# Kernel tuning notes

Measured on AMD Instinct MI355X. Metric: run time of the kernel, lower is better.

## Reference

```python
import jax, jax.numpy as jnp
import numpy as np

NUM_HEADS = 12


def setup_inputs() -> dict:
    key = jax.random.key(0)
    ks = jax.random.split(key, 4)
    N, L, C = 32, 577, 768  # L = 24*24 patches + 1 cls token
    x = jax.random.normal(ks[0], (N, L, C), dtype=jnp.float32)
    w_qkv = jax.random.normal(ks[1], (3 * C, C), dtype=jnp.float32) * 0.02
    w_proj = jax.random.normal(ks[2], (C, C), dtype=jnp.float32) * 0.02
    b_proj = jnp.zeros((C,), dtype=jnp.float32)
    w_dwc = jax.random.normal(ks[3], (C, 1, 3, 3), dtype=jnp.float32) * 0.02
    b_dwc = jnp.zeros((C,), dtype=jnp.float32)
    return {"x": x, "w_qkv": w_qkv, "w_proj": w_proj, "b_proj": b_proj,
            "w_dwc": w_dwc, "b_dwc": b_dwc}


def reference(x, w_qkv, w_proj, b_proj, w_dwc, b_dwc):
    N, L, C = x.shape
    H = NUM_HEADS
    hd = C // H
    h = w = int(L ** 0.5)  # 24; h*w == L-1 (cls token excluded)

    # qkv transform: (N, L, 3C) -> (3, N, H, L, hd)
    qkv = (x @ w_qkv.T).reshape(N, L, 3, H, hd).transpose(2, 0, 3, 1, 4)
    q, k, v = qkv[0], qkv[1], qkv[2]

    # graph-candidate attention (default: scaled dot-product softmax)
    scale = hd ** -0.5
    scores = jnp.einsum('bhqd,bhkd->bhqk', q, k) * scale
    attn = jax.nn.softmax(scores, axis=-1)
    out = jnp.einsum('bhqk,bhkd->bhqd', attn, v)  # (N, H, L, hd)
    out = out.transpose(0, 2, 1, 3).reshape(N, L, C)

    # depthwise conv on v (patch tokens only), NCHW layout
    v_ = v[:, :, 1:, :].transpose(0, 2, 1, 3).reshape(N, h, w, C).transpose(0, 3, 1, 2)
    dwc = jax.lax.conv_general_dilated(
        v_, w_dwc, window_strides=(1, 1), padding=((1, 1), (1, 1)),
        dimension_numbers=('NCHW', 'OIHW', 'NCHW'), feature_group_count=C)
    dwc = dwc + b_dwc[None, :, None, None]
    dwc = dwc.transpose(0, 2, 3, 1).reshape(N, L - 1, C)

    out = out.at[:, 1:, :].add(dwc)
    out = out @ w_proj.T + b_proj
    return out
```

## Files before the change

kernel.cpp:

```cpp
#include <hip/hip_runtime.h>

typedef short bf16x8 __attribute__((ext_vector_type(8)));
typedef float f32x4 __attribute__((ext_vector_type(4)));
typedef unsigned short u16;

#define NB 32
#define LSEQ 577
#define CD 768
#define NH 12
#define HD 64
#define MROWS (NB * LSEQ)
#define LPAD 584

#define GLD16(g, l)                                                    \
  __builtin_amdgcn_global_load_lds(                                    \
      (const __attribute__((address_space(1))) void*)(g),              \
      (__attribute__((address_space(3))) void*)(l), 16, 0, 0)

__device__ __forceinline__ u16 f2bf(float f) {
  union { float f; unsigned u; } v; v.f = f;
  unsigned u = v.u + 0x7fffu + ((v.u >> 16) & 1u);
  return (u16)(u >> 16);
}
__device__ __forceinline__ float bf2f(u16 s) {
  union { unsigned u; float f; } v; v.u = ((unsigned)s) << 16;
  return v.f;
}

__global__ __launch_bounds__(256) void cvt_bf16(
    const float* __restrict__ src, u16* __restrict__ dst, int n4) {
  int i = blockIdx.x * 256 + threadIdx.x;
  if (i < n4) {
    float4 v = reinterpret_cast<const float4*>(src)[i];
    ushort4 o;
    o.x = f2bf(v.x); o.y = f2bf(v.y); o.z = f2bf(v.z); o.w = f2bf(v.w);
    reinterpret_cast<ushort4*>(dst)[i] = o;
  }
}

__global__ __launch_bounds__(256) void qkv_gemm(
    const u16* __restrict__ xb, const u16* __restrict__ wqb,
    u16* __restrict__ qb, u16* __restrict__ kb, u16* __restrict__ vtb) {
  __shared__ __align__(16) u16 As[128 * 32];
  __shared__ __align__(16) u16 Bs[128 * 32];
  const int m0 = blockIdx.x * 128;
  const int n0 = blockIdx.y * 128;
  const int t = threadIdx.x;
  const int lane = t & 63, wid = t >> 6;
  const int wm = wid >> 1, wn = wid & 1;
  const int g = lane >> 4, cl = lane & 15;

  const int srow = wid * 32 + (lane >> 2);
  const int scol = (lane & 3) * 8;
  int ga0 = m0 + srow;      ga0 = ga0 < MROWS ? ga0 : MROWS - 1;
  int ga1 = m0 + srow + 16; ga1 = ga1 < MROWS ? ga1 : MROWS - 1;
  const u16* asrc0 = xb + (size_t)ga0 * CD + scol;
  const u16* asrc1 = xb + (size_t)ga1 * CD + scol;
  const u16* bsrc0 = wqb + (size_t)(n0 + srow) * CD + scol;
  const u16* bsrc1 = wqb + (size_t)(n0 + srow + 16) * CD + scol;
  u16* adst0 = &As[wid * 1024];
  u16* adst1 = &As[wid * 1024 + 512];
  u16* bdst0 = &Bs[wid * 1024];
  u16* bdst1 = &Bs[wid * 1024 + 512];

  const f32x4 fz = {0.f, 0.f, 0.f, 0.f};
  f32x4 acc[4][4];
#pragma unroll
  for (int i = 0; i < 4; ++i)
#pragma unroll
    for (int j = 0; j < 4; ++j) acc[i][j] = fz;

  for (int k0 = 0; k0 < CD; k0 += 32) {
    GLD16(asrc0 + k0, adst0);
    GLD16(asrc1 + k0, adst1);
    GLD16(bsrc0 + k0, bdst0);
    GLD16(bsrc1 + k0, bdst1);
    __syncthreads();
    bf16x8 af[4], bfv[4];
#pragma unroll
    for (int mt = 0; mt < 4; ++mt)
      af[mt] = *reinterpret_cast<const bf16x8*>(&As[(wm * 64 + mt * 16 + cl) * 32 + g * 8]);
#pragma unroll
    for (int nt = 0; nt < 4; ++nt)
      bfv[nt] = *reinterpret_cast<const bf16x8*>(&Bs[(wn * 64 + nt * 16 + cl) * 32 + g * 8]);
#pragma unroll
    for (int mt = 0; mt < 4; ++mt)
#pragma unroll
      for (int nt = 0; nt < 4; ++nt)
        acc[mt][nt] = __builtin_amdgcn_mfma_f32_16x16x32_bf16(af[mt], bfv[nt], acc[mt][nt], 0, 0, 0);
    __syncthreads();
  }

  const int which = n0 / CD;
  const int rem0 = n0 % CD;
#pragma unroll
  for (int mt = 0; mt < 4; ++mt) {
#pragma unroll
    for (int nt = 0; nt < 4; ++nt) {
      int n = rem0 + wn * 64 + nt * 16 + cl;
      int hh = n >> 6, d = n & 63;
#pragma unroll
      for (int r = 0; r < 4; ++r) {
        int m = m0 + wm * 64 + mt * 16 + g * 4 + r;
        if (m < MROWS) {
          int nb = m / LSEQ, l = m % LSEQ;
          if (which == 0)
            qb[(((size_t)nb * NH + hh) * LSEQ + l) * HD + d] = f2bf(acc[mt][nt][r] * 0.125f);
          else if (which == 1)
            kb[(((size_t)nb * NH + hh) * LSEQ + l) * HD + d] = f2bf(acc[mt][nt][r]);
          else
            vtb[(((size_t)nb * NH + hh) * HD + d) * LPAD + l] = f2bf(acc[mt][nt][r]);
        }
      }
    }
  }
}

__global__ __launch_bounds__(256) void attn_fwd(
    const u16* __restrict__ q, const u16* __restrict__ k,
    const u16* __restrict__ vt, u16* __restrict__ y) {
  __shared__ __align__(16) u16 Ks[64 * 72];
  __shared__ __align__(16) u16 Vts[64 * 72];
  __shared__ __align__(16) u16 Ps[4][16 * 72];

  const int qtile = blockIdx.x;
  const int h = blockIdx.y;
  const int nb = blockIdx.z;
  const int t = threadIdx.x;
  const int lane = t & 63, wid = t >> 6;
  const int g = lane >> 4, cl = lane & 15;

  const size_t hoff = ((size_t)nb * NH + h) * LSEQ * HD;
  const u16* qh = q + hoff;
  const u16* kh = k + hoff;
  const u16* vth = vt + ((size_t)nb * NH + h) * HD * LPAD;

  const int qbase = qtile * 64;
  const int qrow = qbase + wid * 16 + cl;
  const int qrc = qrow < LSEQ ? qrow : LSEQ - 1;
  bf16x8 qf0 = *reinterpret_cast<const bf16x8*>(qh + (size_t)qrc * HD + g * 8);
  bf16x8 qf1 = *reinterpret_cast<const bf16x8*>(qh + (size_t)qrc * HD + 32 + g * 8);

  const f32x4 fz = {0.f, 0.f, 0.f, 0.f};
  float mrow = -3.0e38f, lrow = 0.f;
  f32x4 oaccT[4];
#pragma unroll
  for (int dt = 0; dt < 4; ++dt) oaccT[dt] = fz;

  for (int kv = 0; kv < LSEQ; kv += 64) {
#pragma unroll
    for (int i = 0; i < 2; ++i) {
      int cidx = t + 256 * i;
      int row = cidx >> 3, c8 = (cidx & 7) << 3;
      int grow = kv + row;
      uint4 kd = {0, 0, 0, 0};
      if (grow < LSEQ) kd = *reinterpret_cast<const uint4*>(kh + (size_t)grow * HD + c8);
      *reinterpret_cast<uint4*>(&Ks[row * 72 + c8]) = kd;
      uint4 vd = *reinterpret_cast<const uint4*>(vth + (size_t)row * LPAD + kv + c8);
      *reinterpret_cast<uint4*>(&Vts[row * 72 + c8]) = vd;
    }
    __syncthreads();

    f32x4 sT[4];
#pragma unroll
    for (int nt = 0; nt < 4; ++nt) {
      bf16x8 a0 = *reinterpret_cast<const bf16x8*>(&Ks[(nt * 16 + cl) * 72 + g * 8]);
      bf16x8 a1 = *reinterpret_cast<const bf16x8*>(&Ks[(nt * 16 + cl) * 72 + 32 + g * 8]);
      f32x4 s = fz;
      s = __builtin_amdgcn_mfma_f32_16x16x32_bf16(a0, qf0, s, 0, 0, 0);
      s = __builtin_amdgcn_mfma_f32_16x16x32_bf16(a1, qf1, s, 0, 0, 0);
      sT[nt] = s;
    }

#pragma unroll
    for (int nt = 0; nt < 4; ++nt)
#pragma unroll
      for (int r = 0; r < 4; ++r)
        if (kv + nt * 16 + g * 4 + r >= LSEQ) sT[nt][r] = -3.0e38f;

    float pm = -3.0e38f;
#pragma unroll
    for (int nt = 0; nt < 4; ++nt)
#pragma unroll
      for (int r = 0; r < 4; ++r) pm = fmaxf(pm, sT[nt][r]);
    pm = fmaxf(pm, __shfl_xor(pm, 16));
    pm = fmaxf(pm, __shfl_xor(pm, 32));

    float nm = fmaxf(mrow, pm);
    float alpha = __expf(mrow - nm);
    mrow = nm;
    float ps = 0.f;
#pragma unroll
    for (int nt = 0; nt < 4; ++nt)
#pragma unroll
      for (int r = 0; r < 4; ++r) {
        float p = __expf(sT[nt][r] - nm);
        sT[nt][r] = p;
        ps += p;
      }
    ps += __shfl_xor(ps, 16);
    ps += __shfl_xor(ps, 32);
    lrow = lrow * alpha + ps;
#pragma unroll
    for (int dt = 0; dt < 4; ++dt) oaccT[dt] *= alpha;

#pragma unroll
    for (int nt = 0; nt < 4; ++nt) {
      ushort4 p4;
      p4.x = f2bf(sT[nt][0]); p4.y = f2bf(sT[nt][1]);
      p4.z = f2bf(sT[nt][2]); p4.w = f2bf(sT[nt][3]);
      *reinterpret_cast<ushort4*>(&Ps[wid][cl * 72 + nt * 16 + g * 4]) = p4;
    }
    __syncthreads();

#pragma unroll
    for (int kc = 0; kc < 2; ++kc) {
      bf16x8 pa = *reinterpret_cast<const bf16x8*>(&Ps[wid][cl * 72 + kc * 32 + g * 8]);
#pragma unroll
      for (int dt = 0; dt < 4; ++dt) {
        bf16x8 va = *reinterpret_cast<const bf16x8*>(&Vts[(dt * 16 + cl) * 72 + kc * 32 + g * 8]);
        oaccT[dt] = __builtin_amdgcn_mfma_f32_16x16x32_bf16(va, pa, oaccT[dt], 0, 0, 0);
      }
    }
    __syncthreads();
  }

  if (qrow < LSEQ) {
    float inv = 1.f / lrow;
#pragma unroll
    for (int dt = 0; dt < 4; ++dt) {
      ushort4 o4;
      o4.x = f2bf(oaccT[dt][0] * inv); o4.y = f2bf(oaccT[dt][1] * inv);
      o4.z = f2bf(oaccT[dt][2] * inv); o4.w = f2bf(oaccT[dt][3] * inv);
      *reinterpret_cast<ushort4*>(
          &y[((size_t)nb * LSEQ + qrow) * CD + h * HD + dt * 16 + g * 4]) = o4;
    }
  }
}

__global__ __launch_bounds__(256) void dwc_add(
    const u16* __restrict__ vt, const float* __restrict__ wd,
    const float* __restrict__ bd, u16* __restrict__ y) {
  __shared__ u16 V[32 * 588];
  const int d0 = blockIdx.x * 32;
  const int h = blockIdx.y;
  const int nb = blockIdx.z;
  const int t = threadIdx.x;
  const u16* vrow = vt + (((size_t)nb * NH + h) * HD + d0) * LPAD;

  for (int c = t; c < 32 * 73; c += 256) {
    int row = c / 73;
    int k0 = (c - row * 73) * 8;
    uint4 vv = *reinterpret_cast<const uint4*>(vrow + (size_t)row * LPAD + k0);
    const u16* vp = (const u16*)&vv;
    *reinterpret_cast<ushort4*>(&V[row * 588 + k0]) = *(const ushort4*)vp;
    *reinterpret_cast<ushort4*>(&V[row * 588 + k0 + 4]) = *(const ushort4*)(vp + 4);
  }
  __syncthreads();

  const int d = t & 31;
  const int c = h * HD + d0 + d;
  float w9[9];
#pragma unroll
  for (int j = 0; j < 9; ++j) w9[j] = wd[c * 9 + j];
  const float bias = bd[c];
  const u16* Vd = &V[d * 588];

  for (int it = 0; it < 72; ++it) {
    int li = (t >> 5) + it * 8;
    int py = li / 24, px = li - py * 24;
    float acc = bias;
#pragma unroll
    for (int ky = 0; ky < 3; ++ky) {
      int yy = py + ky - 1;
      if (yy < 0 || yy >= 24) continue;
      int base = 1 + yy * 24;
#pragma unroll
      for (int kx = 0; kx < 3; ++kx) {
        int xx = px + kx - 1;
        if (xx < 0 || xx >= 24) continue;
        acc += w9[ky * 3 + kx] * bf2f(Vd[base + xx]);
      }
    }
    size_t yi = ((size_t)nb * LSEQ + 1 + li) * CD + c;
    y[yi] = f2bf(bf2f(y[yi]) + acc);
  }
}

__global__ __launch_bounds__(256) void proj_gemm(
    const u16* __restrict__ yb, const u16* __restrict__ wpb,
    const float* __restrict__ bias, float* __restrict__ out) {
  __shared__ __align__(16) u16 As[128 * 32];
  __shared__ __align__(16) u16 Bs[128 * 32];
  const int m0 = blockIdx.x * 128;
  const int n0 = blockIdx.y * 128;
  const int t = threadIdx.x;
  const int lane = t & 63, wid = t >> 6;
  const int wm = wid >> 1, wn = wid & 1;
  const int g = lane >> 4, cl = lane & 15;

  const int srow = wid * 32 + (lane >> 2);
  const int scol = (lane & 3) * 8;
  int ga0 = m0 + srow;      ga0 = ga0 < MROWS ? ga0 : MROWS - 1;
  int ga1 = m0 + srow + 16; ga1 = ga1 < MROWS ? ga1 : MROWS - 1;
  const u16* asrc0 = yb + (size_t)ga0 * CD + scol;
  const u16* asrc1 = yb + (size_t)ga1 * CD + scol;
  const u16* bsrc0 = wpb + (size_t)(n0 + srow) * CD + scol;
  const u16* bsrc1 = wpb + (size_t)(n0 + srow + 16) * CD + scol;
  u16* adst0 = &As[wid * 1024];
  u16* adst1 = &As[wid * 1024 + 512];
  u16* bdst0 = &Bs[wid * 1024];
  u16* bdst1 = &Bs[wid * 1024 + 512];

  const f32x4 fz = {0.f, 0.f, 0.f, 0.f};
  f32x4 acc[4][4];
#pragma unroll
  for (int i = 0; i < 4; ++i)
#pragma unroll
    for (int j = 0; j < 4; ++j) acc[i][j] = fz;

  for (int k0 = 0; k0 < CD; k0 += 32) {
    GLD16(asrc0 + k0, adst0);
    GLD16(asrc1 + k0, adst1);
    GLD16(bsrc0 + k0, bdst0);
    GLD16(bsrc1 + k0, bdst1);
    __syncthreads();
    bf16x8 af[4], bfv[4];
#pragma unroll
    for (int mt = 0; mt < 4; ++mt)
      af[mt] = *reinterpret_cast<const bf16x8*>(&As[(wm * 64 + mt * 16 + cl) * 32 + g * 8]);
#pragma unroll
    for (int nt = 0; nt < 4; ++nt)
      bfv[nt] = *reinterpret_cast<const bf16x8*>(&Bs[(wn * 64 + nt * 16 + cl) * 32 + g * 8]);
#pragma unroll
    for (int mt = 0; mt < 4; ++mt)
#pragma unroll
      for (int nt = 0; nt < 4; ++nt)
        acc[mt][nt] = __builtin_amdgcn_mfma_f32_16x16x32_bf16(af[mt], bfv[nt], acc[mt][nt], 0, 0, 0);
    __syncthreads();
  }

#pragma unroll
  for (int nt = 0; nt < 4; ++nt) {
    int n = n0 + wn * 64 + nt * 16 + cl;
    float bn = bias[n];
#pragma unroll
    for (int mt = 0; mt < 4; ++mt)
#pragma unroll
      for (int r = 0; r < 4; ++r) {
        int m = m0 + wm * 64 + mt * 16 + g * 4 + r;
        if (m < MROWS) out[(size_t)m * CD + n] = acc[mt][nt][r] + bn;
      }
  }
}

extern "C" void kernel_launch(void* const* d_in, const int* in_sizes, int n_in,
                              void* d_out, int out_size, void* d_ws, size_t ws_size,
                              hipStream_t stream) {
  const float* x = (const float*)d_in[0];
  const float* w_qkv = (const float*)d_in[1];
  const float* w_proj = (const float*)d_in[2];
  const float* b_proj = (const float*)d_in[3];
  const float* w_dwc = (const float*)d_in[4];
  const float* b_dwc = (const float*)d_in[5];
  float* out = (float*)d_out;

  const size_t SEG = (size_t)NB * NH * LSEQ * HD;
  const size_t SEGT = (size_t)NB * NH * HD * LPAD;
  const size_t YN = (size_t)MROWS * CD;
  u16* yb = (u16*)d_ws;
  u16* xb = yb;
  u16* qb = yb + YN;
  u16* kb = qb + SEG;
  u16* vtb = kb + SEG;
  u16* wqb = vtb + SEGT;
  u16* wpb = wqb + (size_t)3 * CD * CD;

  cvt_bf16<<<dim3((int)(YN / 4 / 256)), 256, 0, stream>>>(x, xb, (int)(YN / 4));
  cvt_bf16<<<dim3(3 * CD * CD / 4 / 256), 256, 0, stream>>>(w_qkv, wqb, 3 * CD * CD / 4);
  cvt_bf16<<<dim3(CD * CD / 4 / 256), 256, 0, stream>>>(w_proj, wpb, CD * CD / 4);
  qkv_gemm<<<dim3(145, 18), 256, 0, stream>>>(xb, wqb, qb, kb, vtb);
  attn_fwd<<<dim3(10, 12, 32), 256, 0, stream>>>(qb, kb, vtb, yb);
  dwc_add<<<dim3(2, 12, 32), 256, 0, stream>>>(vtb, w_dwc, b_dwc, yb);
  proj_gemm<<<dim3(145, 6), 256, 0, stream>>>(yb, wpb, b_proj, out);
}
```

Before: 404.0 us.

## Double-buffer LDS in both GEMMs and enlarge QKV tile to 256x256

Both GEMM kernels now keep two LDS buffers and issue the async global-to-LDS loads for the next K slice before running the MFMAs on the current one, with s_setprio raised around the MFMA block. This leaves one barrier per iteration and lets load latency overlap with math. The QKV GEMM also moves to 256x256 tiles with 512 threads (8 waves, 128x64 per wave), which raises operand reuse per LDS load and cuts the grid to 73x9 blocks. In exchange it uses more registers and LDS per block and leaves fewer blocks, so tail effects on the 18464-row M dimension may matter.

Result: no change. 397.3 us (-1.6%).

```diff
diff --git a/kernel.cpp b/kernel.cpp
--- a/kernel.cpp
+++ b/kernel.cpp
@@ -38,72 +38,82 @@
   }
 }
 
-__global__ __launch_bounds__(256) void qkv_gemm(
+__global__ __launch_bounds__(512, 2) void qkv_gemm(
     const u16* __restrict__ xb, const u16* __restrict__ wqb,
     u16* __restrict__ qb, u16* __restrict__ kb, u16* __restrict__ vtb) {
-  __shared__ __align__(16) u16 As[128 * 32];
-  __shared__ __align__(16) u16 Bs[128 * 32];
-  const int m0 = blockIdx.x * 128;
-  const int n0 = blockIdx.y * 128;
+  __shared__ __align__(16) u16 As[2][256 * 32];
+  __shared__ __align__(16) u16 Bs[2][256 * 32];
+  const int m0 = blockIdx.x * 256;
+  const int n0 = blockIdx.y * 256;
   const int t = threadIdx.x;
   const int lane = t & 63, wid = t >> 6;
-  const int wm = wid >> 1, wn = wid & 1;
+  const int wm = wid >> 2, wn = wid & 3;
   const int g = lane >> 4, cl = lane & 15;
 
-  const int srow = wid * 32 + (lane >> 2);
+  const int r16 = lane >> 2;
   const int scol = (lane & 3) * 8;
-  int ga0 = m0 + srow;      ga0 = ga0 < MROWS ? ga0 : MROWS - 1;
-  int ga1 = m0 + srow + 16; ga1 = ga1 < MROWS ? ga1 : MROWS - 1;
-  const u16* asrc0 = xb + (size_t)ga0 * CD + scol;
-  const u16* asrc1 = xb + (size_t)ga1 * CD + scol;
-  const u16* bsrc0 = wqb + (size_t)(n0 + srow) * CD + scol;
-  const u16* bsrc1 = wqb + (size_t)(n0 + srow + 16) * CD + scol;
-  u16* adst0 = &As[wid * 1024];
-  u16* adst1 = &As[wid * 1024 + 512];
-  u16* bdst0 = &Bs[wid * 1024];
-  u16* bdst1 = &Bs[wid * 1024 + 512];
+  const int ra0 = wid * 16 + r16;
+  const int ra1 = 128 + wid * 16 + r16;
+  int gm0 = m0 + ra0; gm0 = gm0 < MROWS ? gm0 : MROWS - 1;
+  int gm1 = m0 + ra1; gm1 = gm1 < MROWS ? gm1 : MROWS - 1;
+  const u16* ax0 = xb + (size_t)gm0 * CD + scol;
+  const u16* ax1 = xb + (size_t)gm1 * CD + scol;
+  const u16* bx0 = wqb + (size_t)(n0 + ra0) * CD + scol;
+  const u16* bx1 = wqb + (size_t)(n0 + ra1) * CD + scol;
 
   const f32x4 fz = {0.f, 0.f, 0.f, 0.f};
-  f32x4 acc[4][4];
-#pragma unroll
-  for (int i = 0; i < 4; ++i)
+  f32x4 acc[8][4];
+#pragma unroll
+  for (int i = 0; i < 8; ++i)
 #pragma unroll
     for (int j = 0; j < 4; ++j) acc[i][j] = fz;
 
-  for (int k0 = 0; k0 < CD; k0 += 32) {
-    GLD16(asrc0 + k0, adst0);
-    GLD16(asrc1 + k0, adst1);
-    GLD16(bsrc0 + k0, bdst0);
-    GLD16(bsrc1 + k0, bdst1);
-    __syncthreads();
-    bf16x8 af[4], bfv[4];
-#pragma unroll
-    for (int mt = 0; mt < 4; ++mt)
-      af[mt] = *reinterpret_cast<const bf16x8*>(&As[(wm * 64 + mt * 16 + cl) * 32 + g * 8]);
+#define QSTAGE(b, kt)                                  \
+  do {                                                 \
+    int kc = (kt) * 32;                                \
+    GLD16(ax0 + kc, &As[b][wid * 512]);                \
+    GLD16(ax1 + kc, &As[b][(wid + 8) * 512]);          \
+    GLD16(bx0 + kc, &Bs[b][wid * 512]);                \
+    GLD16(bx1 + kc, &Bs[b][(wid + 8) * 512]);          \
+  } while (0)
+
+  QSTAGE(0, 0);
+  __syncthreads();
+  int cur = 0;
+  for (int kt = 0; kt < 24; ++kt) {
+    if (kt < 23) QSTAGE(cur ^ 1, kt + 1);
+    bf16x8 af[8], bfv[4];
+#pragma unroll
+    for (int mt = 0; mt < 8; ++mt)
+      af[mt] = *reinterpret_cast<const bf16x8*>(&As[cur][(wm * 128 + mt * 16 + cl) * 32 + g * 8]);
 #pragma unroll
     for (int nt = 0; nt < 4; ++nt)
-      bfv[nt] = *reinterpret_cast<const bf16x8*>(&Bs[(wn * 64 + nt * 16 + cl) * 32 + g * 8]);
-#pragma unroll
-    for (int mt = 0; mt < 4; ++mt)
+      bfv[nt] = *reinterpret_cast<const bf16x8*>(&Bs[cur][(wn * 64 + nt * 16 + cl) * 32 + g * 8]);
+    __builtin_amdgcn_s_setprio(1);
+#pragma unroll
+    for (int mt = 0; mt < 8; ++mt)
 #pragma unroll
       for (int nt = 0; nt < 4; ++nt)
         acc[mt][nt] = __builtin_amdgcn_mfma_f32_16x16x32_bf16(af[mt], bfv[nt], acc[mt][nt], 0, 0, 0);
+    __builtin_amdgcn_s_setprio(0);
     __syncthreads();
-  }
+    cur ^= 1;
+  }
+#undef QSTAGE
 
   const int which = n0 / CD;
   const int rem0 = n0 % CD;
 #pragma unroll
-  for (int mt = 0; mt < 4; ++mt) {
+  for (int mt = 0; mt < 8; ++mt) {
 #pragma unroll
     for (int nt = 0; nt < 4; ++nt) {
-      int n = rem0 + wn * 64 + nt * 16 + cl;
-      int hh = n >> 6, d = n & 63;
+      int rem = rem0 + wn * 64 + nt * 16 + cl;
+      int hh = rem >> 6, d = rem & 63;
 #pragma unroll
       for (int r = 0; r < 4; ++r) {
-        int m = m0 + wm * 64 + mt * 16 + g * 4 + r;
+        int m = m0 + wm * 128 + mt * 16 + g * 4 + r;
         if (m < MROWS) {
-          int nb = m / LSEQ, l = m % LSEQ;
+          int nb = m / LSEQ, l = m - nb * LSEQ;
           if (which == 0)
             qb[(((size_t)nb * NH + hh) * LSEQ + l) * HD + d] = f2bf(acc[mt][nt][r] * 0.125f);
           else if (which == 1)
@@ -290,8 +300,8 @@
 __global__ __launch_bounds__(256) void proj_gemm(
     const u16* __restrict__ yb, const u16* __restrict__ wpb,
     const float* __restrict__ bias, float* __restrict__ out) {
-  __shared__ __align__(16) u16 As[128 * 32];
-  __shared__ __align__(16) u16 Bs[128 * 32];
+  __shared__ __align__(16) u16 As[2][128 * 32];
+  __shared__ __align__(16) u16 Bs[2][128 * 32];
   const int m0 = blockIdx.x * 128;
   const int n0 = blockIdx.y * 128;
   const int t = threadIdx.x;
@@ -307,10 +317,6 @@
   const u16* asrc1 = yb + (size_t)ga1 * CD + scol;
   const u16* bsrc0 = wpb + (size_t)(n0 + srow) * CD + scol;
   const u16* bsrc1 = wpb + (size_t)(n0 + srow + 16) * CD + scol;
-  u16* adst0 = &As[wid * 1024];
-  u16* adst1 = &As[wid * 1024 + 512];
-  u16* bdst0 = &Bs[wid * 1024];
-  u16* bdst1 = &Bs[wid * 1024 + 512];
 
   const f32x4 fz = {0.f, 0.f, 0.f, 0.f};
   f32x4 acc[4][4];
@@ -319,26 +325,38 @@
 #pragma unroll
     for (int j = 0; j < 4; ++j) acc[i][j] = fz;
 
-  for (int k0 = 0; k0 < CD; k0 += 32) {
-    GLD16(asrc0 + k0, adst0);
-    GLD16(asrc1 + k0, adst1);
-    GLD16(bsrc0 + k0, bdst0);
-    GLD16(bsrc1 + k0, bdst1);
-    __syncthreads();
+#define PSTAGE(b, kt)                                   \
+  do {                                                  \
+    int kc = (kt) * 32;                                 \
+    GLD16(asrc0 + kc, &As[b][wid * 1024]);              \
+    GLD16(asrc1 + kc, &As[b][wid * 1024 + 512]);        \
+    GLD16(bsrc0 + kc, &Bs[b][wid * 1024]);              \
+    GLD16(bsrc1 + kc, &Bs[b][wid * 1024 + 512]);        \
+  } while (0)
+
+  PSTAGE(0, 0);
+  __syncthreads();
+  int cur = 0;
+  for (int kt = 0; kt < 24; ++kt) {
+    if (kt < 23) PSTAGE(cur ^ 1, kt + 1);
     bf16x8 af[4], bfv[4];
 #pragma unroll
     for (int mt = 0; mt < 4; ++mt)
-      af[mt] = *reinterpret_cast<const bf16x8*>(&As[(wm * 64 + mt * 16 + cl) * 32 + g * 8]);
+      af[mt] = *reinterpret_cast<const bf16x8*>(&As[cur][(wm * 64 + mt * 16 + cl) * 32 + g * 8]);
 #pragma unroll
     for (int nt = 0; nt < 4; ++nt)
-      bfv[nt] = *reinterpret_cast<const bf16x8*>(&Bs[(wn * 64 + nt * 16 + cl) * 32 + g * 8]);
+      bfv[nt] = *reinterpret_cast<const bf16x8*>(&Bs[cur][(wn * 64 + nt * 16 + cl) * 32 + g * 8]);
+    __builtin_amdgcn_s_setprio(1);
 #pragma unroll
     for (int mt = 0; mt < 4; ++mt)
 #pragma unroll
       for (int nt = 0; nt < 4; ++nt)
         acc[mt][nt] = __builtin_amdgcn_mfma_f32_16x16x32_bf16(af[mt], bfv[nt], acc[mt][nt], 0, 0, 0);
+    __builtin_amdgcn_s_setprio(0);
     __syncthreads();
-  }
+    cur ^= 1;
+  }
+#undef PSTAGE
 
 #pragma unroll
   for (int nt = 0; nt < 4; ++nt) {
@@ -379,7 +397,7 @@
   cvt_bf16<<<dim3((int)(YN / 4 / 256)), 256, 0, stream>>>(x, xb, (int)(YN / 4));
   cvt_bf16<<<dim3(3 * CD * CD / 4 / 256), 256, 0, stream>>>(w_qkv, wqb, 3 * CD * CD / 4);
   cvt_bf16<<<dim3(CD * CD / 4 / 256), 256, 0, stream>>>(w_proj, wpb, CD * CD / 4);
-  qkv_gemm<<<dim3(145, 18), 256, 0, stream>>>(xb, wqb, qb, kb, vtb);
+  qkv_gemm<<<dim3(73, 9), 512, 0, stream>>>(xb, wqb, qb, kb, vtb);
   attn_fwd<<<dim3(10, 12, 32), 256, 0, stream>>>(qb, kb, vtb, yb);
   dwc_add<<<dim3(2, 12, 32), 256, 0, stream>>>(vtb, w_dwc, b_dwc, yb);
   proj_gemm<<<dim3(145, 6), 256, 0, stream>>>(yb, wpb, b_proj, out);
```
